# Kernel optimization log

Measured on AMD Instinct MI355X. Metric: run time of the kernel, lower is better.

The kernel has to match this reference:

```python
import jax, jax.numpy as jnp
import numpy as np

ALPHA = 0.2          # LeakyReLU negative slope
NEG_INF = -9e15      # mask value from the torch code
B, N, F, E, H, S, T, L = 32, 128, 78, 12, 256, 20, 13, 3


def setup_inputs() -> dict:
    key = jax.random.key(0)
    ks = jax.random.split(key, 20)
    sc = 0.05  # param scale
    inp = {
        "node_features": jax.random.normal(ks[0], (B, N, F), jnp.float32),
        "edge_features": jax.random.normal(ks[1], (B, N, N, E), jnp.float32),
        "adj_matrix": jax.random.randint(ks[2], (B, N, N), 0, 2).astype(jnp.int32),
        "scaffold_features": jax.random.normal(ks[3], (B, S), jnp.float32),
        # node projection (Linear F->H, with bias)
        "W_node": jax.random.normal(ks[4], (F, H), jnp.float32) * sc,
        "b_node": jnp.zeros((H,), jnp.float32),
        # stacked GAT layer params: W (H->H, no bias), a (2H->1, no bias)
        "gat_W": jax.random.normal(ks[5], (L, H, H), jnp.float32) * sc,
        "gat_a": jax.random.normal(ks[6], (L, 2 * H), jnp.float32) * sc,
        # scaffold projection (S->H)
        "W_sc": jax.random.normal(ks[7], (S, H), jnp.float32) * sc,
        "b_sc": jnp.zeros((H,), jnp.float32),
        # graph_pooling MLP: H -> H/2 -> H/4 (shared for graph + scaffold paths)
        "gp_w1": jax.random.normal(ks[8], (H, H // 2), jnp.float32) * sc,
        "gp_b1": jnp.zeros((H // 2,), jnp.float32),
        "gp_w2": jax.random.normal(ks[9], (H // 2, H // 4), jnp.float32) * sc,
        "gp_b2": jnp.zeros((H // 4,), jnp.float32),
        # output MLP: (H/4 + H/4) -> H/2 -> T
        "out_w1": jax.random.normal(ks[10], (H // 2, H // 2), jnp.float32) * sc,
        "out_b1": jnp.zeros((H // 2,), jnp.float32),
        "out_w2": jax.random.normal(ks[11], (H // 2, T), jnp.float32) * sc,
        "out_b2": jnp.zeros((T,), jnp.float32),
    }
    return inp


def _gat_stack(x, adj_matrix, gat_W, gat_a):
    # x: (B,N,H); adj: (B,N,N) int
    mask = adj_matrix > 0
    n_layers, _, h_dim = gat_W.shape
    for l in range(n_layers):
        h = jnp.einsum("bnf,fh->bnh", x, gat_W[l])      # (B,N,H)
        a1, a2 = gat_a[l, :h_dim], gat_a[l, h_dim:]
        # a . [h_i ; h_j] == h_i.a1 + h_j.a2 (exact decomposition of the
        # O(N^2, 2H) concat in the torch code)
        s1 = h @ a1                                       # (B,N)
        s2 = h @ a2                                       # (B,N)
        e = jax.nn.leaky_relu(s1[:, :, None] + s2[:, None, :], ALPHA)
        att = jnp.where(mask, e, NEG_INF)                 # (B,N,N)
        att = jax.nn.softmax(att, axis=-1)
        h_prime = jnp.einsum("bij,bjh->bih", att, h)
        x = jax.nn.relu(h_prime)                          # relu after layer (dropout = identity, eval)
    return x


def _pool(z, gp_w1, gp_b1, gp_w2, gp_b2):
    z = jax.nn.relu(z @ gp_w1 + gp_b1)
    return jax.nn.relu(z @ gp_w2 + gp_b2)


def reference(node_features, edge_features, adj_matrix, scaffold_features,
              W_node, b_node, gat_W, gat_a, W_sc, b_sc,
              gp_w1, gp_b1, gp_w2, gp_b2, out_w1, out_b1, out_w2, out_b2):
    # edge_features is accepted but unused in the original forward
    x = node_features @ W_node + b_node                  # (B,N,H)
    x = _gat_stack(x, adj_matrix, gat_W, gat_a)
    graph = x.mean(axis=1)                               # (B,H)
    g = _pool(graph, gp_w1, gp_b1, gp_w2, gp_b2)         # (B,H/4)
    s = _pool(scaffold_features @ W_sc + b_sc, gp_w1, gp_b1, gp_w2, gp_b2)
    c = jnp.concatenate([g, s], axis=-1)                 # (B,H/2)
    hdn = jax.nn.relu(c @ out_w1 + out_b1)
    return hdn @ out_w2 + out_b2                         # (B,T)
```

## Files before the change

kernel.cpp:

```cpp
#include <hip/hip_runtime.h>
#include <hip/hip_bf16.h>

#define NEG_INF -9.0e15f

__device__ __forceinline__ float b2f(__hip_bfloat16 v) { return __bfloat162float(v); }
__device__ __forceinline__ float ldv(const float* p, int i) { return p[i]; }
__device__ __forceinline__ float ldv(const __hip_bfloat16* p, int i) { return __bfloat162float(p[i]); }

__device__ __forceinline__ void unpack8u(uint4 r, float* f) {
    f[0]=__uint_as_float(r.x<<16); f[1]=__uint_as_float(r.x&0xffff0000u);
    f[2]=__uint_as_float(r.y<<16); f[3]=__uint_as_float(r.y&0xffff0000u);
    f[4]=__uint_as_float(r.z<<16); f[5]=__uint_as_float(r.z&0xffff0000u);
    f[6]=__uint_as_float(r.w<<16); f[7]=__uint_as_float(r.w&0xffff0000u);
}
__device__ __forceinline__ void ld8f(const float* p, float* f) {
    const float4* q = (const float4*)p;
    float4 a = q[0], b = q[1];
    f[0]=a.x; f[1]=a.y; f[2]=a.z; f[3]=a.w; f[4]=b.x; f[5]=b.y; f[6]=b.z; f[7]=b.w;
}
__device__ __forceinline__ void ld8f(const __hip_bfloat16* p, float* f) {
    unpack8u(*(const uint4*)p, f);
}

__device__ __forceinline__ void async16(const void* g, void* l) {
    __builtin_amdgcn_global_load_lds(
        (__attribute__((address_space(1))) void*)(g),
        (__attribute__((address_space(3))) void*)(l), 16, 0, 0);
}

__device__ __forceinline__ int sniff(const void* wnode) {
    const unsigned short* w = (const unsigned short*)wnode;
    int lane = threadIdx.x & 63;
    unsigned short u = w[2 * lane];
    int e = (u >> 7) & 0xFF;
    unsigned long long m = __ballot(e >= 100 && e <= 140);
    return __popcll(m) >= 48;
}

template <typename T>
__device__ __forceinline__ void gat_epilogue(
    const T* __restrict__ ga, int tx, int ty, int row0,
    const float* acc0, const float* acc1,
    float* __restrict__ h, float* __restrict__ s1, float* __restrict__ s2) {
    float a1v[8], a2v[8];
    ld8f(ga + 8 * tx, a1v);
    ld8f(ga + 256 + 8 * tx, a2v);
    float d10 = 0.f, d20 = 0.f, d11 = 0.f, d21 = 0.f;
    #pragma unroll
    for (int j = 0; j < 8; ++j) {
        d10 += acc0[j] * a1v[j]; d20 += acc0[j] * a2v[j];
        d11 += acc1[j] * a1v[j]; d21 += acc1[j] * a2v[j];
    }
    #pragma unroll
    for (int off = 1; off < 32; off <<= 1) {
        d10 += __shfl_xor(d10, off, 64); d20 += __shfl_xor(d20, off, 64);
        d11 += __shfl_xor(d11, off, 64); d21 += __shfl_xor(d21, off, 64);
    }
    if (tx == 0) {
        s1[row0 + ty] = d10;     s2[row0 + ty] = d20;
        s1[row0 + ty + 8] = d11; s2[row0 + ty + 8] = d21;
    }
    float4 o00 = {acc0[0], acc0[1], acc0[2], acc0[3]};
    float4 o01 = {acc0[4], acc0[5], acc0[6], acc0[7]};
    float4 o10 = {acc1[0], acc1[1], acc1[2], acc1[3]};
    float4 o11 = {acc1[4], acc1[5], acc1[6], acc1[7]};
    *(float4*)&h[(size_t)(row0 + ty) * 256 + 8 * tx]         = o00;
    *(float4*)&h[(size_t)(row0 + ty) * 256 + 8 * tx + 4]     = o01;
    *(float4*)&h[(size_t)(row0 + ty + 8) * 256 + 8 * tx]     = o10;
    *(float4*)&h[(size_t)(row0 + ty + 8) * 256 + 8 * tx + 4] = o11;
}

__global__ __launch_bounds__(256) void k_gat_h(
    const float* __restrict__ x, const void* __restrict__ gat_W,
    const void* __restrict__ gat_a, int layer,
    const void* __restrict__ nf, const void* __restrict__ Wn,
    const void* __restrict__ bn, int first,
    float* __restrict__ h, float* __restrict__ s1, float* __restrict__ s2) {
    __shared__ float xs[16][256];
    __shared__ float nfs[16][80];
    __shared__ __align__(16) unsigned short Wbuf[2][32 * 256];
    const int t = threadIdx.x;
    const int row0 = blockIdx.x * 16;
    const int tx = t & 31, ty = t >> 5;
    const int isbf = sniff(Wn);

    if (isbf) {
        const __hip_bfloat16* Wl = (const __hip_bfloat16*)gat_W + (size_t)layer * 65536;
        const __hip_bfloat16* ga = (const __hip_bfloat16*)gat_a + (size_t)layer * 512;
        const int ph = blockIdx.x & 7;
        {
            const char* g = (const char*)Wl + ph * 16384;
            char* lb = (char*)&Wbuf[0][0];
            #pragma unroll
            for (int i = 0; i < 4; ++i)
                async16(g + i * 4096 + t * 16, lb + i * 4096 + t * 16);
        }
        if (first) {
            for (int idx = t; idx < 16 * 78; idx += 256) {
                int r = idx / 78, k = idx - r * 78;
                nfs[r][k] = b2f(((const __hip_bfloat16*)nf)[(row0 + r) * 78 + k]);
            }
            __syncthreads();
            const __hip_bfloat16* Wnb = (const __hip_bfloat16*)Wn;
            float p0[8], p1[8];
            ld8f((const __hip_bfloat16*)bn + 8 * tx, p0);
            #pragma unroll
            for (int j = 0; j < 8; ++j) p1[j] = p0[j];
            for (int k = 0; k < 78; ++k) {
                float w8[8]; ld8f(Wnb + k * 256 + 8 * tx, w8);
                float xv0 = nfs[ty][k], xv1 = nfs[ty + 8][k];
                #pragma unroll
                for (int j = 0; j < 8; ++j) {
                    p0[j] += xv0 * w8[j];
                    p1[j] += xv1 * w8[j];
                }
            }
            #pragma unroll
            for (int j = 0; j < 8; ++j) {
                xs[ty][8 * tx + j] = p0[j];
                xs[ty + 8][8 * tx + j] = p1[j];
            }
            __syncthreads();
        } else {
            #pragma unroll
            for (int i = 0; i < 4; ++i) {
                int idx = t + 256 * i;
                int r = idx >> 6, c4 = idx & 63;
                ((float4*)&xs[r][0])[c4] = ((const float4*)&x[(size_t)(row0 + r) * 256])[c4];
            }
            __syncthreads();
        }
        float acc0[8], acc1[8];
        #pragma unroll
        for (int j = 0; j < 8; ++j) { acc0[j] = 0.f; acc1[j] = 0.f; }
        for (int c = 0; c < 8; ++c) {
            if (c < 7) {
                const char* g = (const char*)Wl + (((c + 1 + ph) & 7) * 16384);
                char* lb = (char*)&Wbuf[(c + 1) & 1][0];
                #pragma unroll
                for (int i = 0; i < 4; ++i)
                    async16(g + i * 4096 + t * 16, lb + i * 4096 + t * 16);
            }
            const unsigned short* Wc = &Wbuf[c & 1][0];
            const int kb = ((c + ph) & 7) * 32;
            #pragma unroll 2
            for (int k0 = 0; k0 < 32; k0 += 4) {
                float4 xa = *(const float4*)&xs[ty][kb + k0];
                float4 xb = *(const float4*)&xs[ty + 8][kb + k0];
                float xav[4] = {xa.x, xa.y, xa.z, xa.w};
                float xbv[4] = {xb.x, xb.y, xb.z, xb.w};
                #pragma unroll
                for (int kk = 0; kk < 4; ++kk) {
                    uint4 wv = *(const uint4*)&Wc[(k0 + kk) * 256 + 8 * tx];
                    float w8[8]; unpack8u(wv, w8);
                    #pragma unroll
                    for (int j = 0; j < 8; ++j) {
                        acc0[j] += xav[kk] * w8[j];
                        acc1[j] += xbv[kk] * w8[j];
                    }
                }
            }
            __syncthreads();
        }
        gat_epilogue<__hip_bfloat16>(ga, tx, ty, row0, acc0, acc1, h, s1, s2);
    } else {
        const float* Wl = (const float*)gat_W + (size_t)layer * 65536;
        const float* ga = (const float*)gat_a + (size_t)layer * 512;
        if (first) {
            for (int idx = t; idx < 16 * 78; idx += 256) {
                int r = idx / 78, k = idx - r * 78;
                nfs[r][k] = ((const float*)nf)[(row0 + r) * 78 + k];
            }
            __syncthreads();
            float p0[8], p1[8];
            ld8f((const float*)bn + 8 * tx, p0);
            #pragma unroll
            for (int j = 0; j < 8; ++j) p1[j] = p0[j];
            for (int k = 0; k < 78; ++k) {
                float w8[8]; ld8f((const float*)Wn + k * 256 + 8 * tx, w8);
                float xv0 = nfs[ty][k], xv1 = nfs[ty + 8][k];
                #pragma unroll
                for (int j = 0; j < 8; ++j) { p0[j] += xv0 * w8[j]; p1[j] += xv1 * w8[j]; }
            }
            #pragma unroll
            for (int j = 0; j < 8; ++j) {
                xs[ty][8 * tx + j] = p0[j];
                xs[ty + 8][8 * tx + j] = p1[j];
            }
            __syncthreads();
        } else {
            #pragma unroll
            for (int i = 0; i < 4; ++i) {
                int idx = t + 256 * i;
                int r = idx >> 6, c4 = idx & 63;
                ((float4*)&xs[r][0])[c4] = ((const float4*)&x[(size_t)(row0 + r) * 256])[c4];
            }
            __syncthreads();
        }
        float acc0[8], acc1[8];
        #pragma unroll
        for (int j = 0; j < 8; ++j) { acc0[j] = 0.f; acc1[j] = 0.f; }
        for (int k = 0; k < 256; ++k) {
            float w8[8]; ld8f(Wl + k * 256 + 8 * tx, w8);
            float xv0 = xs[ty][k], xv1 = xs[ty + 8][k];
            #pragma unroll
            for (int j = 0; j < 8; ++j) { acc0[j] += xv0 * w8[j]; acc1[j] += xv1 * w8[j]; }
        }
        gat_epilogue<float>(ga, tx, ty, row0, acc0, acc1, h, s1, s2);
    }
}

__global__ __launch_bounds__(256) void k_attn(
    const float* __restrict__ h, const float* __restrict__ s1,
    const float* __restrict__ s2, const int* __restrict__ adj,
    float* __restrict__ x, float* __restrict__ gpart, int do_pool) {
    __shared__ float att_t[128][10];
    __shared__ __align__(16) float hbuf[2][32 * 256];
    __shared__ float pool_red[4][256];
    int blk = blockIdx.x, b = blk >> 4, i0 = (blk & 15) << 3;
    int t = threadIdx.x, w = t >> 6, lane = t & 63;
    const char* hbytes = (const char*)(h + (size_t)b * 32768);
    const int ph = blk & 3;
    {
        char* lb = (char*)&hbuf[0][0];
        const char* g = hbytes + ph * 32768;
        #pragma unroll
        for (int i = 0; i < 8; ++i)
            async16(g + i * 4096 + t * 16, lb + i * 4096 + t * 16);
    }
    {
        int c0 = lane, c1 = lane + 64;
        int ir0 = i0 + 2 * w, ir1 = ir0 + 1;
        const int* a0 = adj + (size_t)(b * 128 + ir0) * 128;
        const int* a1 = adj + (size_t)(b * 128 + ir1) * 128;
        int m00 = a0[c0], m01 = a0[c1], m10 = a1[c0], m11 = a1[c1];
        float sv0 = s1[b * 128 + ir0], sv1 = s1[b * 128 + ir1];
        float t0 = s2[b * 128 + c0],   t1 = s2[b * 128 + c1];
        float e00 = sv0 + t0; e00 = (e00 >= 0.f) ? e00 : 0.2f * e00;
        float e01 = sv0 + t1; e01 = (e01 >= 0.f) ? e01 : 0.2f * e01;
        float e10 = sv1 + t0; e10 = (e10 >= 0.f) ? e10 : 0.2f * e10;
        float e11 = sv1 + t1; e11 = (e11 >= 0.f) ? e11 : 0.2f * e11;
        float v00 = (m00 > 0) ? e00 : NEG_INF;
        float v01 = (m01 > 0) ? e01 : NEG_INF;
        float v10 = (m10 > 0) ? e10 : NEG_INF;
        float v11 = (m11 > 0) ? e11 : NEG_INF;
        float mx0 = fmaxf(v00, v01), mx1 = fmaxf(v10, v11);
        #pragma unroll
        for (int off = 1; off < 64; off <<= 1) {
            mx0 = fmaxf(mx0, __shfl_xor(mx0, off, 64));
            mx1 = fmaxf(mx1, __shfl_xor(mx1, off, 64));
        }
        float p00 = __expf(v00 - mx0), p01 = __expf(v01 - mx0);
        float p10 = __expf(v10 - mx1), p11 = __expf(v11 - mx1);
        float s0 = p00 + p01, ss1 = p10 + p11;
        #pragma unroll
        for (int off = 1; off < 64; off <<= 1) {
            s0  += __shfl_xor(s0, off, 64);
            ss1 += __shfl_xor(ss1, off, 64);
        }
        float inv0 = 1.0f / s0, inv1 = 1.0f / ss1;
        att_t[c0][2 * w]     = p00 * inv0;
        att_t[c1][2 * w]     = p01 * inv0;
        att_t[c0][2 * w + 1] = p10 * inv1;
        att_t[c1][2 * w + 1] = p11 * inv1;
    }
    __syncthreads();
    int tx = t & 63, ty = t >> 6;
    float acc0[4] = {0.f, 0.f, 0.f, 0.f}, acc1[4] = {0.f, 0.f, 0.f, 0.f};
    for (int c = 0; c < 4; ++c) {
        if (c < 3) {
            char* lb = (char*)&hbuf[(c + 1) & 1][0];
            const char* g = hbytes + (((c + 1 + ph) & 3) * 32768);
            #pragma unroll
            for (int i = 0; i < 8; ++i)
                async16(g + i * 4096 + t * 16, lb + i * 4096 + t * 16);
        }
        const float* hc = &hbuf[c & 1][0];
        const int jb = ((c + ph) & 3) * 32;
        #pragma unroll 4
        for (int jj = 0; jj < 32; ++jj) {
            float4 hv = *(const float4*)&hc[jj * 256 + 4 * tx];
            float2 ap = *(const float2*)&att_t[jb + jj][2 * ty];
            acc0[0] += ap.x * hv.x; acc0[1] += ap.x * hv.y;
            acc0[2] += ap.x * hv.z; acc0[3] += ap.x * hv.w;
            acc1[0] += ap.y * hv.x; acc1[1] += ap.y * hv.y;
            acc1[2] += ap.y * hv.z; acc1[3] += ap.y * hv.w;
        }
        __syncthreads();
    }
    if (!do_pool) {
        float4 o0 = {fmaxf(acc0[0],0.f), fmaxf(acc0[1],0.f), fmaxf(acc0[2],0.f), fmaxf(acc0[3],0.f)};
        float4 o1 = {fmaxf(acc1[0],0.f), fmaxf(acc1[1],0.f), fmaxf(acc1[2],0.f), fmaxf(acc1[3],0.f)};
        *(float4*)&x[(size_t)(b * 128 + i0 + 2 * ty)     * 256 + 4 * tx] = o0;
        *(float4*)&x[(size_t)(b * 128 + i0 + 2 * ty + 1) * 256 + 4 * tx] = o1;
    } else {
        float4 pr = {(fmaxf(acc0[0],0.f) + fmaxf(acc1[0],0.f)) * (1.f/128.f),
                     (fmaxf(acc0[1],0.f) + fmaxf(acc1[1],0.f)) * (1.f/128.f),
// ... 130 lines not shown
    }
    __syncthreads();
    if (t < 13) {
        if (isbf) ((__hip_bfloat16*)out)[b * 13 + t] = __float2bfloat16(outv[t]);
        else      ((float*)out)[b * 13 + t] = outv[t];
    }
}

extern "C" void kernel_launch(void* const* d_in, const int* in_sizes, int n_in,
                              void* d_out, int out_size, void* d_ws, size_t ws_size,
                              hipStream_t stream) {
    (void)in_sizes; (void)n_in; (void)out_size; (void)ws_size;
    const void* nf     = d_in[0];
    const int*  adj    = (const int*)d_in[2];
    const void* scaf   = d_in[3];
    const void* W_node = d_in[4];
    const void* b_node = d_in[5];
    const void* gat_W  = d_in[6];
    const void* gat_a  = d_in[7];
    const void* W_sc   = d_in[8];
    const void* b_sc   = d_in[9];
    const void* gp_w1  = d_in[10];
    const void* gp_b1  = d_in[11];
    const void* gp_w2  = d_in[12];
    const void* gp_b2  = d_in[13];
    const void* out_w1 = d_in[14];
    const void* out_b1 = d_in[15];
    const void* out_w2 = d_in[16];
    const void* out_b2 = d_in[17];

    float* ws    = (float*)d_ws;
    float* x     = ws;
    float* h     = ws + 1048576;
    float* s1    = ws + 2097152;
    float* s2    = s1 + 4096;
    float* gpart = s2 + 4096;

    for (int l = 0; l < 3; ++l) {
        k_gat_h<<<256, 256, 0, stream>>>(x, gat_W, gat_a, l,
                                         nf, W_node, b_node, (l == 0) ? 1 : 0,
                                         h, s1, s2);
        k_attn<<<512, 256, 0, stream>>>(h, s1, s2, adj, x, gpart, (l == 2) ? 1 : 0);
    }
    k_head<<<32, 256, 0, stream>>>(gpart, scaf, W_sc, b_sc, gp_w1, gp_b1, gp_w2, gp_b2,
                                   out_w1, out_b1, out_w2, out_b2, d_out, W_node);
}
```

Baseline: 228.2 us.

## Use bf16 MFMA with hi/lo split for GAT projection and node embedding

Replaces the scalar FMA projection x@W in the GAT kernel with MFMA 16x16x32 bf16 instructions. Activations are split into bf16 hi and lo parts so that fp32-level accuracy is kept, and the node embedding also runs on MFMA. A new pre-pass kernel transposes the layer and node weights into an N-major layout so they can be fed to the MFMA. The grid is doubled by splitting the output columns into two halves, and the partial attention scores are summed in the attention kernel. This adds an extra launch plus transpose work, and uses two MFMAs per tile.

```diff
diff --git a/kernel.cpp b/kernel.cpp
--- a/kernel.cpp
+++ b/kernel.cpp
@@ -2,25 +2,32 @@
 #include <hip/hip_bf16.h>
 
 #define NEG_INF -9.0e15f
+
+using u16 = unsigned short;
+typedef float f32x4 __attribute__((ext_vector_type(4)));
+typedef short s16x8 __attribute__((ext_vector_type(8)));
 
 __device__ __forceinline__ float b2f(__hip_bfloat16 v) { return __bfloat162float(v); }
 __device__ __forceinline__ float ldv(const float* p, int i) { return p[i]; }
 __device__ __forceinline__ float ldv(const __hip_bfloat16* p, int i) { return __bfloat162float(p[i]); }
-
-__device__ __forceinline__ void unpack8u(uint4 r, float* f) {
+__device__ __forceinline__ float bu2f(u16 u) { return __uint_as_float(((unsigned)u) << 16); }
+__device__ __forceinline__ u16 f2bu(float v) {
+    __hip_bfloat16 h = __float2bfloat16(v);
+    return *(u16*)&h;
+}
+
+__device__ __forceinline__ void ld8f(const float* p, float* f) {
+    const float4* q = (const float4*)p;
+    float4 a = q[0], b = q[1];
+    f[0]=a.x; f[1]=a.y; f[2]=a.z; f[3]=a.w; f[4]=b.x; f[5]=b.y; f[6]=b.z; f[7]=b.w;
+}
+__device__ __forceinline__ void ld8f(const __hip_bfloat16* p, float* f) {
+    uint4 r = *(const uint4*)p;
     f[0]=__uint_as_float(r.x<<16); f[1]=__uint_as_float(r.x&0xffff0000u);
     f[2]=__uint_as_float(r.y<<16); f[3]=__uint_as_float(r.y&0xffff0000u);
     f[4]=__uint_as_float(r.z<<16); f[5]=__uint_as_float(r.z&0xffff0000u);
     f[6]=__uint_as_float(r.w<<16); f[7]=__uint_as_float(r.w&0xffff0000u);
 }
-__device__ __forceinline__ void ld8f(const float* p, float* f) {
-    const float4* q = (const float4*)p;
-    float4 a = q[0], b = q[1];
-    f[0]=a.x; f[1]=a.y; f[2]=a.z; f[3]=a.w; f[4]=b.x; f[5]=b.y; f[6]=b.z; f[7]=b.w;
-}
-__device__ __forceinline__ void ld8f(const __hip_bfloat16* p, float* f) {
-    unpack8u(*(const uint4*)p, f);
-}
 
 __device__ __forceinline__ void async16(const void* g, void* l) {
     __builtin_amdgcn_global_load_lds(
@@ -28,191 +35,268 @@
         (__attribute__((address_space(3))) void*)(l), 16, 0, 0);
 }
 
+__device__ __forceinline__ f32x4 mfma16(s16x8 a, s16x8 b, f32x4 c) {
+    return __builtin_amdgcn_mfma_f32_16x16x32_bf16(a, b, c, 0, 0, 0);
+}
+
 __device__ __forceinline__ int sniff(const void* wnode) {
-    const unsigned short* w = (const unsigned short*)wnode;
+    const u16* w = (const u16*)wnode;
     int lane = threadIdx.x & 63;
-    unsigned short u = w[2 * lane];
+    u16 u = w[2 * lane];
     int e = (u >> 7) & 0xFF;
     unsigned long long m = __ballot(e >= 100 && e <= 140);
     return __popcll(m) >= 48;
 }
 
-template <typename T>
-__device__ __forceinline__ void gat_epilogue(
-    const T* __restrict__ ga, int tx, int ty, int row0,
-    const float* acc0, const float* acc1,
-    float* __restrict__ h, float* __restrict__ s1, float* __restrict__ s2) {
-    float a1v[8], a2v[8];
-    ld8f(ga + 8 * tx, a1v);
-    ld8f(ga + 256 + 8 * tx, a2v);
-    float d10 = 0.f, d20 = 0.f, d11 = 0.f, d21 = 0.f;
-    #pragma unroll
-    for (int j = 0; j < 8; ++j) {
-        d10 += acc0[j] * a1v[j]; d20 += acc0[j] * a2v[j];
-        d11 += acc1[j] * a1v[j]; d21 += acc1[j] * a2v[j];
-    }
-    #pragma unroll
-    for (int off = 1; off < 32; off <<= 1) {
-        d10 += __shfl_xor(d10, off, 64); d20 += __shfl_xor(d20, off, 64);
-        d11 += __shfl_xor(d11, off, 64); d21 += __shfl_xor(d21, off, 64);
-    }
-    if (tx == 0) {
-        s1[row0 + ty] = d10;     s2[row0 + ty] = d20;
-        s1[row0 + ty + 8] = d11; s2[row0 + ty + 8] = d21;
-    }
-    float4 o00 = {acc0[0], acc0[1], acc0[2], acc0[3]};
-    float4 o01 = {acc0[4], acc0[5], acc0[6], acc0[7]};
-    float4 o10 = {acc1[0], acc1[1], acc1[2], acc1[3]};
-    float4 o11 = {acc1[4], acc1[5], acc1[6], acc1[7]};
-    *(float4*)&h[(size_t)(row0 + ty) * 256 + 8 * tx]         = o00;
-    *(float4*)&h[(size_t)(row0 + ty) * 256 + 8 * tx + 4]     = o01;
-    *(float4*)&h[(size_t)(row0 + ty + 8) * 256 + 8 * tx]     = o10;
-    *(float4*)&h[(size_t)(row0 + ty + 8) * 256 + 8 * tx + 4] = o11;
-}
-
-__global__ __launch_bounds__(256) void k_gat_h(
-    const float* __restrict__ x, const void* __restrict__ gat_W,
-    const void* __restrict__ gat_a, int layer,
-    const void* __restrict__ nf, const void* __restrict__ Wn,
-    const void* __restrict__ bn, int first,
-    float* __restrict__ h, float* __restrict__ s1, float* __restrict__ s2) {
-    __shared__ float xs[16][256];
-    __shared__ float nfs[16][80];
-    __shared__ __align__(16) unsigned short Wbuf[2][32 * 256];
+__global__ __launch_bounds__(256) void k_wt(
+    const void* __restrict__ gat_W, const void* __restrict__ W_node,
+    u16* __restrict__ Wt, u16* __restrict__ Wnt) {
+    if (!sniff(W_node)) return;
+    int b = blockIdx.x, t = threadIdx.x;
+    if (b < 24) {
+        int l = b >> 3, nb = (b & 7) * 32;
+        const u16* Ws = (const u16*)gat_W + (size_t)l * 65536;
+        u16* Wd = Wt + (size_t)l * 65536;
+        int n = nb + (t & 31), kc = t >> 5;
+        u16 tmp[32];
+        #pragma unroll 8
+        for (int kk = 0; kk < 32; ++kk) tmp[kk] = Ws[(kc * 32 + kk) * 256 + n];
+        #pragma unroll
+        for (int kk = 0; kk < 32; ++kk) Wd[n * 256 + kc * 32 + kk] = tmp[kk];
+    } else {
+        int nb = (b - 24) * 128;
+        const u16* Ws = (const u16*)W_node;
+        int n = nb + (t >> 1), hf = t & 1;
+        for (int kk = 0; kk < 48; ++kk) {
+            int k = hf * 48 + kk;
+            Wnt[n * 96 + k] = (k < 78) ? Ws[k * 256 + n] : (u16)0;
+        }
+    }
+}
+
+__global__ __launch_bounds__(256) void k_gat(
+    const float* __restrict__ x, const u16* __restrict__ Wt,
+    const void* __restrict__ gat_W_raw, const void* __restrict__ gat_a,
+    int layer, const void* __restrict__ nf, const u16* __restrict__ Wnt,
+    const void* __restrict__ Wn_raw, const void* __restrict__ bn, int first,
+    float* __restrict__ h, float* __restrict__ sp1, float* __restrict__ sp2) {
+    __shared__ __align__(16) char smem[36864];
+    u16* xs_hi = (u16*)smem;
+    u16* xs_lo = (u16*)(smem + 8448);
+    char* wbB  = smem + 16896;
+    u16* nfs   = (u16*)(smem + 33280);
+    float* sred = (float*)(smem + 36352);
+
     const int t = threadIdx.x;
-    const int row0 = blockIdx.x * 16;
-    const int tx = t & 31, ty = t >> 5;
-    const int isbf = sniff(Wn);
+    const int w = t >> 6, lane = t & 63, quad = lane >> 4, l16 = lane & 15;
+    const int rb = blockIdx.x >> 1, nh = blockIdx.x & 1;
+    const int row0 = rb * 16, n0 = nh * 128;
+    const int isbf = sniff(Wn_raw);
 
     if (isbf) {
-        const __hip_bfloat16* Wl = (const __hip_bfloat16*)gat_W + (size_t)layer * 65536;
-        const __hip_bfloat16* ga = (const __hip_bfloat16*)gat_a + (size_t)layer * 512;
-        const int ph = blockIdx.x & 7;
+        if (first) {
+            const u16* nfu = (const u16*)nf;
+            for (int i = t; i < 16 * 96; i += 256) {
+                int r = i / 96, k = i - r * 96;
+                nfs[i] = (k < 78) ? nfu[(row0 + r) * 78 + k] : (u16)0;
+            }
+            __syncthreads();
+            f32x4 pa[4];
+            const u16* bnu = (const u16*)bn;
+            #pragma unroll
+            for (int tt = 0; tt < 4; ++tt) {
+                float bv = bu2f(bnu[w * 64 + tt * 16 + l16]);
+                pa[tt] = (f32x4){bv, bv, bv, bv};
+            }
+            for (int c = 0; c < 3; ++c) {
+                #pragma unroll
+                for (int j = 0; j < 4; ++j) {
+                    int dest = (w * 4 + j) * 4096 + lane * 16;
+                    int nl = (w * 4 + j) * 64 + (lane >> 2);
+                    const char* src = (const char*)(Wnt + nl * 96 + c * 32 + (lane & 3) * 8);
+                    async16(src, wbB + dest);
+                }
+                __syncthreads();
+                s16x8 a = *(const s16x8*)(nfs + l16 * 96 + c * 32 + quad * 8);
+                #pragma unroll
+                for (int tt = 0; tt < 4; ++tt) {
+                    s16x8 bfr = *(const s16x8*)((const u16*)wbB +
+                                 (w * 64 + tt * 16 + l16) * 32 + quad * 8);
+                    pa[tt] = mfma16(a, bfr, pa[tt]);
+                }
+                __syncthreads();
+            }
+            #pragma unroll
+            for (int tt = 0; tt < 4; ++tt) {
+                #pragma unroll
+                for (int r = 0; r < 4; ++r) {
+                    float v = pa[tt][r];
+                    u16 hi = f2bu(v);
+                    u16 lo = f2bu(v - bu2f(hi));
+                    int idx = (quad * 4 + r) * 264 + w * 64 + tt * 16 + l16;
+                    xs_hi[idx] = hi;
+                    xs_lo[idx] = lo;
+                }
+            }
+        } else {
+            int row = t >> 4, kb = (t & 15) * 16;
+            const float4* xp = (const float4*)(x + (size_t)(row0 + row) * 256 + kb);
+            float v[16];
+            #pragma unroll
+            for (int q = 0; q < 4; ++q) {
+                float4 f = xp[q];
+                v[4*q] = f.x; v[4*q+1] = f.y; v[4*q+2] = f.z; v[4*q+3] = f.w;
+            }
+            unsigned hp[8], lp[8];
+            #pragma unroll
+            for (int i = 0; i < 8; ++i) {
+                u16 h0 = f2bu(v[2*i]),   h1 = f2bu(v[2*i+1]);
+                u16 l0 = f2bu(v[2*i] - bu2f(h0)), l1 = f2bu(v[2*i+1] - bu2f(h1));
+                hp[i] = (unsigned)h0 | ((unsigned)h1 << 16);
+                lp[i] = (unsigned)l0 | ((unsigned)l1 << 16);
+            }
+            uint4* dh = (uint4*)(xs_hi + row * 264 + kb);
+            uint4* dl = (uint4*)(xs_lo + row * 264 + kb);
+            dh[0] = (uint4){hp[0], hp[1], hp[2], hp[3]};
+            dh[1] = (uint4){hp[4], hp[5], hp[6], hp[7]};
+            dl[0] = (uint4){lp[0], lp[1], lp[2], lp[3]};
+            dl[1] = (uint4){lp[4], lp[5], lp[6], lp[7]};
+        }
+        const u16* Wtl = Wt + (size_t)layer * 65536;
         {
-            const char* g = (const char*)Wl + ph * 16384;
-            char* lb = (char*)&Wbuf[0][0];
-            #pragma unroll
-            for (int i = 0; i < 4; ++i)
-                async16(g + i * 4096 + t * 16, lb + i * 4096 + t * 16);
-        }
+            #pragma unroll
+            for (int j = 0; j < 2; ++j) {
+                int dest = (w * 2 + j) * 2048 + lane * 16;
+                int nl = (w * 2 + j) * 32 + (lane >> 2);
+                const char* src = (const char*)(Wtl + (size_t)(n0 + nl) * 256 + (lane & 3) * 8);
+                async16(src, wbB + dest);
+            }
+        }
+        f32x4 ac0 = {0.f, 0.f, 0.f, 0.f}, ac1 = {0.f, 0.f, 0.f, 0.f};
+        for (int c = 0; c < 8; ++c) {
+            __syncthreads();
+            if (c < 7) {
+                #pragma unroll
+                for (int j = 0; j < 2; ++j) {
+                    int dest = (((c + 1) & 1) * 8192) + (w * 2 + j) * 2048 + lane * 16;
+                    int nl = (w * 2 + j) * 32 + (lane >> 2);
+                    const char* src = (const char*)(Wtl + (size_t)(n0 + nl) * 256 +
+                                                    (c + 1) * 32 + (lane & 3) * 8);
+                    async16(src, wbB + dest);
+                }
+            }
+            const u16* wb = (const u16*)(wbB + (c & 1) * 8192);
+            s16x8 ah = *(const s16x8*)(xs_hi + l16 * 264 + c * 32 + quad * 8);
+            s16x8 al = *(const s16x8*)(xs_lo + l16 * 264 + c * 32 + quad * 8);
+            s16x8 b0 = *(const s16x8*)(wb + (w * 32 + l16) * 32 + quad * 8);
+            s16x8 b1 = *(const s16x8*)(wb + (w * 32 + 16 + l16) * 32 + quad * 8);
+            ac0 = mfma16(ah, b0, ac0);
+            ac0 = mfma16(al, b0, ac0);
+            ac1 = mfma16(ah, b1, ac1);
+            ac1 = mfma16(al, b1, ac1);
+        }
+        const __hip_bfloat16* gab = (const __hip_bfloat16*)gat_a + (size_t)layer * 512;
+        int c0 = n0 + w * 32 + l16, c1 = c0 + 16;
+        float a10 = b2f(gab[c0]), a11 = b2f(gab[c1]);
+        float a20 = b2f(gab[256 + c0]), a21 = b2f(gab[256 + c1]);
+        float p1[4], p2[4];
+        #pragma unroll
+        for (int r = 0; r < 4; ++r) {
+            p1[r] = ac0[r] * a10 + ac1[r] * a11;
+            p2[r] = ac0[r] * a20 + ac1[r] * a21;
+            #pragma unroll
+            for (int off = 1; off < 16; off <<= 1) {
+                p1[r] += __shfl_xor(p1[r], off, 64);
+                p2[r] += __shfl_xor(p2[r], off, 64);
+            }
+        }
+        if (l16 == 0) {
+            #pragma unroll
+            for (int r = 0; r < 4; ++r) {
+                sred[w * 16 + quad * 4 + r] = p1[r];
+                sred[64 + w * 16 + quad * 4 + r] = p2[r];
+            }
+        }
+        #pragma unroll
+        for (int r = 0; r < 4; ++r) {
+            int gr = row0 + quad * 4 + r;
+            h[(size_t)gr * 256 + n0 + w * 32 + l16]      = ac0[r];
+            h[(size_t)gr * 256 + n0 + w * 32 + 16 + l16] = ac1[r];
+        }
+        __syncthreads();
+        if (t < 16) {
+            sp1[nh * 4096 + row0 + t] = sred[t] + sred[16 + t] + sred[32 + t] + sred[48 + t];
+            sp2[nh * 4096 + row0 + t] = sred[64 + t] + sred[80 + t] + sred[96 + t] + sred[112 + t];
+        }
+    } else {
+        float* xsf = (float*)smem;
+        const float* Wl = (const float*)gat_W_raw + (size_t)layer * 65536;
+        const float* gaf = (const float*)gat_a + (size_t)layer * 512;
         if (first) {
-            for (int idx = t; idx < 16 * 78; idx += 256) {
-                int r = idx / 78, k = idx - r * 78;
-                nfs[r][k] = b2f(((const __hip_bfloat16*)nf)[(row0 + r) * 78 + k]);
+            float* nfsf = (float*)(smem + 16896);
+            const float* nff = (const float*)nf;
+            for (int i = t; i < 16 * 78; i += 256) {
+                int r = i / 78, k = i - r * 78;
+                nfsf[r * 80 + k] = nff[(row0 + r) * 78 + k];
             }
             __syncthreads();
-            const __hip_bfloat16* Wnb = (const __hip_bfloat16*)Wn;
-            float p0[8], p1[8];
-            ld8f((const __hip_bfloat16*)bn + 8 * tx, p0);
-            #pragma unroll
-            for (int j = 0; j < 8; ++j) p1[j] = p0[j];
+            int row = t >> 4, cb = (t & 15) * 16;
+            const float* Wnf = (const float*)Wn_raw;
+            const float* bnf = (const float*)bn;
+            float acc[16];
+            #pragma unroll
+            for (int j = 0; j < 16; ++j) acc[j] = bnf[cb + j];
             for (int k = 0; k < 78; ++k) {
-                float w8[8]; ld8f(Wnb + k * 256 + 8 * tx, w8);
-                float xv0 = nfs[ty][k], xv1 = nfs[ty + 8][k];
+                float xv = nfsf[row * 80 + k];
                 #pragma unroll
-                for (int j = 0; j < 8; ++j) {
-                    p0[j] += xv0 * w8[j];
-                    p1[j] += xv1 * w8[j];
-                }
-            }
-            #pragma unroll
-            for (int j = 0; j < 8; ++j) {
-                xs[ty][8 * tx + j] = p0[j];
-                xs[ty + 8][8 * tx + j] = p1[j];
-            }
+                for (int j = 0; j < 16; ++j) acc[j] += xv * Wnf[k * 256 + cb + j];
+            }
+            #pragma unroll
+            for (int j = 0; j < 16; ++j) xsf[row * 256 + cb + j] = acc[j];
             __syncthreads();
         } else {
-            #pragma unroll
-            for (int i = 0; i < 4; ++i) {
-                int idx = t + 256 * i;
-                int r = idx >> 6, c4 = idx & 63;
-                ((float4*)&xs[r][0])[c4] = ((const float4*)&x[(size_t)(row0 + r) * 256])[c4];
+            for (int i = t; i < 16 * 64; i += 256) {
+                int r = i >> 6, c4 = i & 63;
+                ((float4*)(xsf + r * 256))[c4] =
+                    ((const float4*)(x + (size_t)(row0 + r) * 256))[c4];
             }
             __syncthreads();
         }
-        float acc0[8], acc1[8];
-        #pragma unroll
-        for (int j = 0; j < 8; ++j) { acc0[j] = 0.f; acc1[j] = 0.f; }
-        for (int c = 0; c < 8; ++c) {
-            if (c < 7) {
-                const char* g = (const char*)Wl + (((c + 1 + ph) & 7) * 16384);
-                char* lb = (char*)&Wbuf[(c + 1) & 1][0];
-                #pragma unroll
-                for (int i = 0; i < 4; ++i)
-                    async16(g + i * 4096 + t * 16, lb + i * 4096 + t * 16);
-            }
-            const unsigned short* Wc = &Wbuf[c & 1][0];
-            const int kb = ((c + ph) & 7) * 32;
-            #pragma unroll 2
-            for (int k0 = 0; k0 < 32; k0 += 4) {
-                float4 xa = *(const float4*)&xs[ty][kb + k0];
-                float4 xb = *(const float4*)&xs[ty + 8][kb + k0];
-                float xav[4] = {xa.x, xa.y, xa.z, xa.w};
-                float xbv[4] = {xb.x, xb.y, xb.z, xb.w};
-                #pragma unroll
-                for (int kk = 0; kk < 4; ++kk) {
-                    uint4 wv = *(const uint4*)&Wc[(k0 + kk) * 256 + 8 * tx];
-                    float w8[8]; unpack8u(wv, w8);
-                    #pragma unroll
-                    for (int j = 0; j < 8; ++j) {
-                        acc0[j] += xav[kk] * w8[j];
-                        acc1[j] += xbv[kk] * w8[j];
-                    }
-                }
-            }
-            __syncthreads();
-        }
-        gat_epilogue<__hip_bfloat16>(ga, tx, ty, row0, acc0, acc1, h, s1, s2);
-    } else {
-        const float* Wl = (const float*)gat_W + (size_t)layer * 65536;
-        const float* ga = (const float*)gat_a + (size_t)layer * 512;
-        if (first) {
-            for (int idx = t; idx < 16 * 78; idx += 256) {
-                int r = idx / 78, k = idx - r * 78;
-                nfs[r][k] = ((const float*)nf)[(row0 + r) * 78 + k];
-            }
-            __syncthreads();
-            float p0[8], p1[8];
-            ld8f((const float*)bn + 8 * tx, p0);
-            #pragma unroll
-            for (int j = 0; j < 8; ++j) p1[j] = p0[j];
-            for (int k = 0; k < 78; ++k) {
-                float w8[8]; ld8f((const float*)Wn + k * 256 + 8 * tx, w8);
-                float xv0 = nfs[ty][k], xv1 = nfs[ty + 8][k];
-                #pragma unroll
-                for (int j = 0; j < 8; ++j) { p0[j] += xv0 * w8[j]; p1[j] += xv1 * w8[j]; }
-            }
-            #pragma unroll
-            for (int j = 0; j < 8; ++j) {
-                xs[ty][8 * tx + j] = p0[j];
-                xs[ty + 8][8 * tx + j] = p1[j];
-            }
-            __syncthreads();
-        } else {
-            #pragma unroll
-            for (int i = 0; i < 4; ++i) {
-                int idx = t + 256 * i;
-                int r = idx >> 6, c4 = idx & 63;
-                ((float4*)&xs[r][0])[c4] = ((const float4*)&x[(size_t)(row0 + r) * 256])[c4];
-            }
-            __syncthreads();
-        }
-        float acc0[8], acc1[8];
-        #pragma unroll
-        for (int j = 0; j < 8; ++j) { acc0[j] = 0.f; acc1[j] = 0.f; }
+        int ty = t >> 4, col0 = n0 + (t & 15) * 8;
+        float acc[8];
+        #pragma unroll
+        for (int j = 0; j < 8; ++j) acc[j] = 0.f;
         for (int k = 0; k < 256; ++k) {
-            float w8[8]; ld8f(Wl + k * 256 + 8 * tx, w8);
-            float xv0 = xs[ty][k], xv1 = xs[ty + 8][k];
-            #pragma unroll
-            for (int j = 0; j < 8; ++j) { acc0[j] += xv0 * w8[j]; acc1[j] += xv1 * w8[j]; }
-        }
-        gat_epilogue<float>(ga, tx, ty, row0, acc0, acc1, h, s1, s2);
+            float xv = xsf[ty * 256 + k];
+            float w8[8]; ld8f(Wl + k * 256 + col0, w8);
+            #pragma unroll
+            for (int j = 0; j < 8; ++j) acc[j] += xv * w8[j];
+        }
+        float d1 = 0.f, d2 = 0.f;
+        #pragma unroll
+        for (int j = 0; j < 8; ++j) {
+            d1 += acc[j] * gaf[col0 + j];
+            d2 += acc[j] * gaf[256 + col0 + j];
+        }
+        #pragma unroll
+        for (int off = 1; off < 16; off <<= 1) {
+            d1 += __shfl_xor(d1, off, 64);
+            d2 += __shfl_xor(d2, off, 64);
+        }
+        if ((lane & 15) == 0) { sred[ty] = d1; sred[32 + ty] = d2; }
+        #pragma unroll
+        for (int j = 0; j < 8; ++j) h[(size_t)(row0 + ty) * 256 + col0 + j] = acc[j];
+        __syncthreads();
+        if (t < 16) {
+            sp1[nh * 4096 + row0 + t] = sred[t];
+            sp2[nh * 4096 + row0 + t] = sred[32 + t];
+        }
     }
 }
 
 __global__ __launch_bounds__(256) void k_attn(
-    const float* __restrict__ h, const float* __restrict__ s1,
-    const float* __restrict__ s2, const int* __restrict__ adj,
+    const float* __restrict__ h, const float* __restrict__ sp1,
+    const float* __restrict__ sp2, const int* __restrict__ adj,
     float* __restrict__ x, float* __restrict__ gpart, int do_pool) {
     __shared__ float att_t[128][10];
     __shared__ __align__(16) float hbuf[2][32 * 256];
@@ -234,8 +318,10 @@
         const int* a0 = adj + (size_t)(b * 128 + ir0) * 128;
         const int* a1 = adj + (size_t)(b * 128 + ir1) * 128;
         int m00 = a0[c0], m01 = a0[c1], m10 = a1[c0], m11 = a1[c1];
-        float sv0 = s1[b * 128 + ir0], sv1 = s1[b * 128 + ir1];
-        float t0 = s2[b * 128 + c0],   t1 = s2[b * 128 + c1];
+        float sv0 = sp1[b * 128 + ir0] + sp1[4096 + b * 128 + ir0];
+        float sv1 = sp1[b * 128 + ir1] + sp1[4096 + b * 128 + ir1];
+        float t0 = sp2[b * 128 + c0] + sp2[4096 + b * 128 + c0];
+        float t1 = sp2[b * 128 + c1] + sp2[4096 + b * 128 + c1];
         float e00 = sv0 + t0; e00 = (e00 >= 0.f) ? e00 : 0.2f * e00;
         float e01 = sv0 + t1; e01 = (e01 >= 0.f) ? e01 : 0.2f * e01;
         float e10 = sv1 + t0; e10 = (e10 >= 0.f) ? e10 : 0.2f * e10;
@@ -459,15 +545,18 @@
     float* ws    = (float*)d_ws;
     float* x     = ws;
     float* h     = ws + 1048576;
-    float* s1    = ws + 2097152;
-    float* s2    = s1 + 4096;
-    float* gpart = s2 + 4096;
-
+    float* sp1   = ws + 2097152;
+    float* sp2   = sp1 + 8192;
+    float* gpart = sp2 + 8192;
+    u16*   Wt    = (u16*)(gpart + 131072);
+    u16*   Wnt   = Wt + 196608;
+
+    k_wt<<<26, 256, 0, stream>>>(gat_W, W_node, Wt, Wnt);
     for (int l = 0; l < 3; ++l) {
-        k_gat_h<<<256, 256, 0, stream>>>(x, gat_W, gat_a, l,
-                                         nf, W_node, b_node, (l == 0) ? 1 : 0,
-                                         h, s1, s2);
-        k_attn<<<512, 256, 0, stream>>>(h, s1, s2, adj, x, gpart, (l == 2) ? 1 : 0);
+        k_gat<<<512, 256, 0, stream>>>(x, Wt, gat_W, gat_a, l,
+                                       nf, Wnt, W_node, b_node, (l == 0) ? 1 : 0,
+                                       h, sp1, sp2);
+        k_attn<<<512, 256, 0, stream>>>(h, sp1, sp2, adj, x, gpart, (l == 2) ? 1 : 0);
     }
     k_head<<<32, 256, 0, stream>>>(gpart, scaf, W_sc, b_sc, gp_w1, gp_b1, gp_w2, gp_b2,
                                    out_w1, out_b1, out_w2, out_b2, d_out, W_node);
```

Measured after the change: 285.2 us. +25.0%, slower.

## Replicate bf16 weights into 8 copies and shrink GAT projection tiles to 8 rows

Applied to the files above, without the earlier changes.

Adds a kernel that copies gat_W and W_node into eight replicated buffers in workspace, so that blocks read from different copies (selected by bx&7) and contention on the same addresses is reduced. The projection kernel now handles 8 rows per block across 512 blocks and streams weights straight from global memory instead of double-buffering them in LDS through async loads. Activations are stored transposed in shared memory. Costs are one extra launch with a copy every call, and each weight value is reused over fewer rows, so each block issues more global reads.

```diff
diff --git a/kernel.cpp b/kernel.cpp
--- a/kernel.cpp
+++ b/kernel.cpp
@@ -2,25 +2,12 @@
 #include <hip/hip_bf16.h>
 
 #define NEG_INF -9.0e15f
+
+using u16 = unsigned short;
 
 __device__ __forceinline__ float b2f(__hip_bfloat16 v) { return __bfloat162float(v); }
 __device__ __forceinline__ float ldv(const float* p, int i) { return p[i]; }
 __device__ __forceinline__ float ldv(const __hip_bfloat16* p, int i) { return __bfloat162float(p[i]); }
-
-__device__ __forceinline__ void unpack8u(uint4 r, float* f) {
-    f[0]=__uint_as_float(r.x<<16); f[1]=__uint_as_float(r.x&0xffff0000u);
-    f[2]=__uint_as_float(r.y<<16); f[3]=__uint_as_float(r.y&0xffff0000u);
-    f[4]=__uint_as_float(r.z<<16); f[5]=__uint_as_float(r.z&0xffff0000u);
-    f[6]=__uint_as_float(r.w<<16); f[7]=__uint_as_float(r.w&0xffff0000u);
-}
-__device__ __forceinline__ void ld8f(const float* p, float* f) {
-    const float4* q = (const float4*)p;
-    float4 a = q[0], b = q[1];
-    f[0]=a.x; f[1]=a.y; f[2]=a.z; f[3]=a.w; f[4]=b.x; f[5]=b.y; f[6]=b.z; f[7]=b.w;
-}
-__device__ __forceinline__ void ld8f(const __hip_bfloat16* p, float* f) {
-    unpack8u(*(const uint4*)p, f);
-}
 
 __device__ __forceinline__ void async16(const void* g, void* l) {
     __builtin_amdgcn_global_load_lds(
@@ -29,184 +16,191 @@
 }
 
 __device__ __forceinline__ int sniff(const void* wnode) {
-    const unsigned short* w = (const unsigned short*)wnode;
+    const u16* w = (const u16*)wnode;
     int lane = threadIdx.x & 63;
-    unsigned short u = w[2 * lane];
+    u16 u = w[2 * lane];
     int e = (u >> 7) & 0xFF;
     unsigned long long m = __ballot(e >= 100 && e <= 140);
     return __popcll(m) >= 48;
 }
 
-template <typename T>
-__device__ __forceinline__ void gat_epilogue(
-    const T* __restrict__ ga, int tx, int ty, int row0,
-    const float* acc0, const float* acc1,
+__global__ __launch_bounds__(256) void k_rep(
+    const void* __restrict__ gat_W, const void* __restrict__ W_node,
+    u16* __restrict__ Wrep, u16* __restrict__ Wnrep) {
+    if (!sniff(W_node)) return;
+    int b = blockIdx.x, t = threadIdx.x;
+    if (b < 384) {
+        int c = b / 48, idx = (b % 48) * 256 + t;
+        ((uint4*)(Wrep + (size_t)c * 196608))[idx] = ((const uint4*)gat_W)[idx];
+    } else {
+        int bb = b - 384;
+        int c = bb / 5, idx = (bb % 5) * 256 + t;
+        if (idx < 1248)
+            ((uint4*)(Wnrep + (size_t)c * 19968))[idx] = ((const uint4*)W_node)[idx];
+    }
+}
+
+__global__ __launch_bounds__(256) void k_gat(
+    const float* __restrict__ x, const void* __restrict__ gat_W,
+    const u16* __restrict__ Wrep, const void* __restrict__ gat_a, int layer,
+    const void* __restrict__ nf, const void* __restrict__ Wn_raw,
+    const u16* __restrict__ Wnrep, const void* __restrict__ bn, int first,
     float* __restrict__ h, float* __restrict__ s1, float* __restrict__ s2) {
-    float a1v[8], a2v[8];
-    ld8f(ga + 8 * tx, a1v);
-    ld8f(ga + 256 + 8 * tx, a2v);
-    float d10 = 0.f, d20 = 0.f, d11 = 0.f, d21 = 0.f;
-    #pragma unroll
-    for (int j = 0; j < 8; ++j) {
-        d10 += acc0[j] * a1v[j]; d20 += acc0[j] * a2v[j];
-        d11 += acc1[j] * a1v[j]; d21 += acc1[j] * a2v[j];
-    }
-    #pragma unroll
-    for (int off = 1; off < 32; off <<= 1) {
-        d10 += __shfl_xor(d10, off, 64); d20 += __shfl_xor(d20, off, 64);
-        d11 += __shfl_xor(d11, off, 64); d21 += __shfl_xor(d21, off, 64);
-    }
-    if (tx == 0) {
-        s1[row0 + ty] = d10;     s2[row0 + ty] = d20;
-        s1[row0 + ty + 8] = d11; s2[row0 + ty + 8] = d21;
-    }
-    float4 o00 = {acc0[0], acc0[1], acc0[2], acc0[3]};
-    float4 o01 = {acc0[4], acc0[5], acc0[6], acc0[7]};
-    float4 o10 = {acc1[0], acc1[1], acc1[2], acc1[3]};
-    float4 o11 = {acc1[4], acc1[5], acc1[6], acc1[7]};
-    *(float4*)&h[(size_t)(row0 + ty) * 256 + 8 * tx]         = o00;
-    *(float4*)&h[(size_t)(row0 + ty) * 256 + 8 * tx + 4]     = o01;
-    *(float4*)&h[(size_t)(row0 + ty + 8) * 256 + 8 * tx]     = o10;
-    *(float4*)&h[(size_t)(row0 + ty + 8) * 256 + 8 * tx + 4] = o11;
-}
-
-__global__ __launch_bounds__(256) void k_gat_h(
-    const float* __restrict__ x, const void* __restrict__ gat_W,
-    const void* __restrict__ gat_a, int layer,
-    const void* __restrict__ nf, const void* __restrict__ Wn,
-    const void* __restrict__ bn, int first,
-    float* __restrict__ h, float* __restrict__ s1, float* __restrict__ s2) {
-    __shared__ float xs[16][256];
-    __shared__ float nfs[16][80];
-    __shared__ __align__(16) unsigned short Wbuf[2][32 * 256];
+    __shared__ float xsT[256 * 10];
     const int t = threadIdx.x;
-    const int row0 = blockIdx.x * 16;
-    const int tx = t & 31, ty = t >> 5;
-    const int isbf = sniff(Wn);
+    const int bx = blockIdx.x;
+    const int row0 = bx * 8;
+    const int tx = t & 63, w = t >> 6;
+    const int isbf = sniff(Wn_raw);
+    const int c0 = 4 * tx;
+
+    float acc0[4], acc1[4];
 
     if (isbf) {
-        const __hip_bfloat16* Wl = (const __hip_bfloat16*)gat_W + (size_t)layer * 65536;
+        if (first) {
+            const u16* nfu = (const u16*)nf;
+            for (int i = t; i < 624; i += 256) {
+                int r = i / 78, k = i - r * 78;
+                xsT[k * 10 + r] = __uint_as_float(((unsigned)nfu[(row0 + r) * 78 + k]) << 16);
+            }
+            __syncthreads();
+            const u16* Wnl = Wnrep + (size_t)(bx & 7) * 19968;
+            const __hip_bfloat16* bnb = (const __hip_bfloat16*)bn;
+            #pragma unroll
+            for (int j = 0; j < 4; ++j) { acc0[j] = b2f(bnb[c0 + j]); acc1[j] = acc0[j]; }
+            #pragma unroll 2
+            for (int k = 0; k < 78; ++k) {
+                uint2 wv = *(const uint2*)(Wnl + k * 256 + c0);
+                float w0 = __uint_as_float(wv.x << 16);
+                float w1 = __uint_as_float(wv.x & 0xffff0000u);
+                float w2 = __uint_as_float(wv.y << 16);
+                float w3 = __uint_as_float(wv.y & 0xffff0000u);
+                float2 xp = *(const float2*)&xsT[k * 10 + 2 * w];
+                acc0[0] += xp.x * w0; acc0[1] += xp.x * w1;
+                acc0[2] += xp.x * w2; acc0[3] += xp.x * w3;
+                acc1[0] += xp.y * w0; acc1[1] += xp.y * w1;
+                acc1[2] += xp.y * w2; acc1[3] += xp.y * w3;
+            }
+            __syncthreads();
+            #pragma unroll
+            for (int j = 0; j < 4; ++j) {
+                xsT[(c0 + j) * 10 + 2 * w]     = acc0[j];
+                xsT[(c0 + j) * 10 + 2 * w + 1] = acc1[j];
+            }
+            __syncthreads();
+        } else {
+            int r = t >> 5, cb = (t & 31) * 8;
+            const float4* xp = (const float4*)(x + (size_t)(row0 + r) * 256 + cb);
+            float4 f0 = xp[0], f1 = xp[1];
+            xsT[(cb + 0) * 10 + r] = f0.x; xsT[(cb + 1) * 10 + r] = f0.y;
+            xsT[(cb + 2) * 10 + r] = f0.z; xsT[(cb + 3) * 10 + r] = f0.w;
+            xsT[(cb + 4) * 10 + r] = f1.x; xsT[(cb + 5) * 10 + r] = f1.y;
+            xsT[(cb + 6) * 10 + r] = f1.z; xsT[(cb + 7) * 10 + r] = f1.w;
+            __syncthreads();
+        }
+        const u16* Wl = Wrep + (size_t)(bx & 7) * 196608 + (size_t)layer * 65536;
+        #pragma unroll
+        for (int j = 0; j < 4; ++j) { acc0[j] = 0.f; acc1[j] = 0.f; }
+        #pragma unroll 4
+        for (int k = 0; k < 256; ++k) {
+            uint2 wv = *(const uint2*)(Wl + k * 256 + c0);
+            float w0 = __uint_as_float(wv.x << 16);
+            float w1 = __uint_as_float(wv.x & 0xffff0000u);
+            float w2 = __uint_as_float(wv.y << 16);
+            float w3 = __uint_as_float(wv.y & 0xffff0000u);
+            float2 xp = *(const float2*)&xsT[k * 10 + 2 * w];
+            acc0[0] += xp.x * w0; acc0[1] += xp.x * w1;
+            acc0[2] += xp.x * w2; acc0[3] += xp.x * w3;
+            acc1[0] += xp.y * w0; acc1[1] += xp.y * w1;
+            acc1[2] += xp.y * w2; acc1[3] += xp.y * w3;
+        }
         const __hip_bfloat16* ga = (const __hip_bfloat16*)gat_a + (size_t)layer * 512;
-        const int ph = blockIdx.x & 7;
-        {
-            const char* g = (const char*)Wl + ph * 16384;
-            char* lb = (char*)&Wbuf[0][0];
+        float d10 = 0.f, d20 = 0.f, d11 = 0.f, d21 = 0.f;
+        #pragma unroll
+        for (int j = 0; j < 4; ++j) {
+            float a1v = b2f(ga[c0 + j]), a2v = b2f(ga[256 + c0 + j]);
+            d10 += acc0[j] * a1v; d20 += acc0[j] * a2v;
+            d11 += acc1[j] * a1v; d21 += acc1[j] * a2v;
+        }
+        #pragma unroll
+        for (int off = 1; off < 64; off <<= 1) {
+            d10 += __shfl_xor(d10, off, 64); d20 += __shfl_xor(d20, off, 64);
+            d11 += __shfl_xor(d11, off, 64); d21 += __shfl_xor(d21, off, 64);
+        }
+        if (tx == 0) {
+            s1[row0 + 2 * w] = d10;     s2[row0 + 2 * w] = d20;
+            s1[row0 + 2 * w + 1] = d11; s2[row0 + 2 * w + 1] = d21;
+        }
+        *(float4*)&h[(size_t)(row0 + 2 * w) * 256 + c0]     = (float4){acc0[0], acc0[1], acc0[2], acc0[3]};
+        *(float4*)&h[(size_t)(row0 + 2 * w + 1) * 256 + c0] = (float4){acc1[0], acc1[1], acc1[2], acc1[3]};
+    } else {
+        const float* Wlf = (const float*)gat_W + (size_t)layer * 65536;
+        const float* gaf = (const float*)gat_a + (size_t)layer * 512;
+        if (first) {
+            const float* nff = (const float*)nf;
+            for (int i = t; i < 624; i += 256) {
+                int r = i / 78, k = i - r * 78;
+                xsT[k * 10 + r] = nff[(row0 + r) * 78 + k];
+            }
+            __syncthreads();
+            const float* Wnf = (const float*)Wn_raw;
+            const float* bnf = (const float*)bn;
             #pragma unroll
-            for (int i = 0; i < 4; ++i)
-                async16(g + i * 4096 + t * 16, lb + i * 4096 + t * 16);
-        }
-        if (first) {
-            for (int idx = t; idx < 16 * 78; idx += 256) {
-                int r = idx / 78, k = idx - r * 78;
-                nfs[r][k] = b2f(((const __hip_bfloat16*)nf)[(row0 + r) * 78 + k]);
-            }
-            __syncthreads();
-            const __hip_bfloat16* Wnb = (const __hip_bfloat16*)Wn;
-            float p0[8], p1[8];
-            ld8f((const __hip_bfloat16*)bn + 8 * tx, p0);
+            for (int j = 0; j < 4; ++j) { acc0[j] = bnf[c0 + j]; acc1[j] = acc0[j]; }
+            for (int k = 0; k < 78; ++k) {
+                float4 wf = *(const float4*)(Wnf + k * 256 + c0);
+                float2 xp = *(const float2*)&xsT[k * 10 + 2 * w];
+                acc0[0] += xp.x * wf.x; acc0[1] += xp.x * wf.y;
+                acc0[2] += xp.x * wf.z; acc0[3] += xp.x * wf.w;
+                acc1[0] += xp.y * wf.x; acc1[1] += xp.y * wf.y;
+                acc1[2] += xp.y * wf.z; acc1[3] += xp.y * wf.w;
+            }
+            __syncthreads();
             #pragma unroll
-            for (int j = 0; j < 8; ++j) p1[j] = p0[j];
-            for (int k = 0; k < 78; ++k) {
-                float w8[8]; ld8f(Wnb + k * 256 + 8 * tx, w8);
-                float xv0 = nfs[ty][k], xv1 = nfs[ty + 8][k];
-                #pragma unroll
-                for (int j = 0; j < 8; ++j) {
-                    p0[j] += xv0 * w8[j];
-                    p1[j] += xv1 * w8[j];
-                }
-            }
-            #pragma unroll
-            for (int j = 0; j < 8; ++j) {
-                xs[ty][8 * tx + j] = p0[j];
-                xs[ty + 8][8 * tx + j] = p1[j];
+            for (int j = 0; j < 4; ++j) {
+                xsT[(c0 + j) * 10 + 2 * w]     = acc0[j];
+                xsT[(c0 + j) * 10 + 2 * w + 1] = acc1[j];
             }
             __syncthreads();
         } else {
-            #pragma unroll
-            for (int i = 0; i < 4; ++i) {
-                int idx = t + 256 * i;
-                int r = idx >> 6, c4 = idx & 63;
-                ((float4*)&xs[r][0])[c4] = ((const float4*)&x[(size_t)(row0 + r) * 256])[c4];
-            }
-            __syncthreads();
-        }
-        float acc0[8], acc1[8];
-        #pragma unroll
-        for (int j = 0; j < 8; ++j) { acc0[j] = 0.f; acc1[j] = 0.f; }
-        for (int c = 0; c < 8; ++c) {
-            if (c < 7) {
-                const char* g = (const char*)Wl + (((c + 1 + ph) & 7) * 16384);
-                char* lb = (char*)&Wbuf[(c + 1) & 1][0];
-                #pragma unroll
-                for (int i = 0; i < 4; ++i)
-                    async16(g + i * 4096 + t * 16, lb + i * 4096 + t * 16);
-            }
-            const unsigned short* Wc = &Wbuf[c & 1][0];
-            const int kb = ((c + ph) & 7) * 32;
-            #pragma unroll 2
-            for (int k0 = 0; k0 < 32; k0 += 4) {
-                float4 xa = *(const float4*)&xs[ty][kb + k0];
-                float4 xb = *(const float4*)&xs[ty + 8][kb + k0];
-                float xav[4] = {xa.x, xa.y, xa.z, xa.w};
-                float xbv[4] = {xb.x, xb.y, xb.z, xb.w};
-                #pragma unroll
-                for (int kk = 0; kk < 4; ++kk) {
-                    uint4 wv = *(const uint4*)&Wc[(k0 + kk) * 256 + 8 * tx];
-                    float w8[8]; unpack8u(wv, w8);
-                    #pragma unroll
-                    for (int j = 0; j < 8; ++j) {
-                        acc0[j] += xav[kk] * w8[j];
-                        acc1[j] += xbv[kk] * w8[j];
-                    }
-                }
-            }
-            __syncthreads();
-        }
-        gat_epilogue<__hip_bfloat16>(ga, tx, ty, row0, acc0, acc1, h, s1, s2);
-    } else {
-        const float* Wl = (const float*)gat_W + (size_t)layer * 65536;
-        const float* ga = (const float*)gat_a + (size_t)layer * 512;
-        if (first) {
-            for (int idx = t; idx < 16 * 78; idx += 256) {
-                int r = idx / 78, k = idx - r * 78;
-                nfs[r][k] = ((const float*)nf)[(row0 + r) * 78 + k];
-            }
-            __syncthreads();
-            float p0[8], p1[8];
-            ld8f((const float*)bn + 8 * tx, p0);
-            #pragma unroll
-            for (int j = 0; j < 8; ++j) p1[j] = p0[j];
-            for (int k = 0; k < 78; ++k) {
-                float w8[8]; ld8f((const float*)Wn + k * 256 + 8 * tx, w8);
-                float xv0 = nfs[ty][k], xv1 = nfs[ty + 8][k];
-                #pragma unroll
-                for (int j = 0; j < 8; ++j) { p0[j] += xv0 * w8[j]; p1[j] += xv1 * w8[j]; }
-            }
-            #pragma unroll
-            for (int j = 0; j < 8; ++j) {
-                xs[ty][8 * tx + j] = p0[j];
-                xs[ty + 8][8 * tx + j] = p1[j];
-            }
-            __syncthreads();
-        } else {
-            #pragma unroll
-            for (int i = 0; i < 4; ++i) {
-                int idx = t + 256 * i;
-                int r = idx >> 6, c4 = idx & 63;
-                ((float4*)&xs[r][0])[c4] = ((const float4*)&x[(size_t)(row0 + r) * 256])[c4];
-            }
-            __syncthreads();
-        }
-        float acc0[8], acc1[8];
-        #pragma unroll
-        for (int j = 0; j < 8; ++j) { acc0[j] = 0.f; acc1[j] = 0.f; }
+            int r = t >> 5, cb = (t & 31) * 8;
+            const float4* xp = (const float4*)(x + (size_t)(row0 + r) * 256 + cb);
+            float4 f0 = xp[0], f1 = xp[1];
+            xsT[(cb + 0) * 10 + r] = f0.x; xsT[(cb + 1) * 10 + r] = f0.y;
+            xsT[(cb + 2) * 10 + r] = f0.z; xsT[(cb + 3) * 10 + r] = f0.w;
+            xsT[(cb + 4) * 10 + r] = f1.x; xsT[(cb + 5) * 10 + r] = f1.y;
+            xsT[(cb + 6) * 10 + r] = f1.z; xsT[(cb + 7) * 10 + r] = f1.w;
+            __syncthreads();
+        }
+        #pragma unroll
+        for (int j = 0; j < 4; ++j) { acc0[j] = 0.f; acc1[j] = 0.f; }
+        #pragma unroll 4
         for (int k = 0; k < 256; ++k) {
-            float w8[8]; ld8f(Wl + k * 256 + 8 * tx, w8);
-            float xv0 = xs[ty][k], xv1 = xs[ty + 8][k];
-            #pragma unroll
-            for (int j = 0; j < 8; ++j) { acc0[j] += xv0 * w8[j]; acc1[j] += xv1 * w8[j]; }
-        }
-        gat_epilogue<float>(ga, tx, ty, row0, acc0, acc1, h, s1, s2);
+            float4 wf = *(const float4*)(Wlf + k * 256 + c0);
+            float2 xp = *(const float2*)&xsT[k * 10 + 2 * w];
+            acc0[0] += xp.x * wf.x; acc0[1] += xp.x * wf.y;
+            acc0[2] += xp.x * wf.z; acc0[3] += xp.x * wf.w;
+            acc1[0] += xp.y * wf.x; acc1[1] += xp.y * wf.y;
+            acc1[2] += xp.y * wf.z; acc1[3] += xp.y * wf.w;
+        }
+        float d10 = 0.f, d20 = 0.f, d11 = 0.f, d21 = 0.f;
+        #pragma unroll
+        for (int j = 0; j < 4; ++j) {
+            float a1v = gaf[c0 + j], a2v = gaf[256 + c0 + j];
+            d10 += acc0[j] * a1v; d20 += acc0[j] * a2v;
+            d11 += acc1[j] * a1v; d21 += acc1[j] * a2v;
+        }
+        #pragma unroll
+        for (int off = 1; off < 64; off <<= 1) {
+            d10 += __shfl_xor(d10, off, 64); d20 += __shfl_xor(d20, off, 64);
+            d11 += __shfl_xor(d11, off, 64); d21 += __shfl_xor(d21, off, 64);
+        }
+        if (tx == 0) {
+            s1[row0 + 2 * w] = d10;     s2[row0 + 2 * w] = d20;
+            s1[row0 + 2 * w + 1] = d11; s2[row0 + 2 * w + 1] = d21;
+        }
+        *(float4*)&h[(size_t)(row0 + 2 * w) * 256 + c0]     = (float4){acc0[0], acc0[1], acc0[2], acc0[3]};
+        *(float4*)&h[(size_t)(row0 + 2 * w + 1) * 256 + c0] = (float4){acc1[0], acc1[1], acc1[2], acc1[3]};
     }
 }
 
@@ -229,13 +223,13 @@
             async16(g + i * 4096 + t * 16, lb + i * 4096 + t * 16);
     }
     {
-        int c0 = lane, c1 = lane + 64;
+        int cc0 = lane, cc1 = lane + 64;
         int ir0 = i0 + 2 * w, ir1 = ir0 + 1;
         const int* a0 = adj + (size_t)(b * 128 + ir0) * 128;
         const int* a1 = adj + (size_t)(b * 128 + ir1) * 128;
-        int m00 = a0[c0], m01 = a0[c1], m10 = a1[c0], m11 = a1[c1];
+        int m00 = a0[cc0], m01 = a0[cc1], m10 = a1[cc0], m11 = a1[cc1];
         float sv0 = s1[b * 128 + ir0], sv1 = s1[b * 128 + ir1];
-        float t0 = s2[b * 128 + c0],   t1 = s2[b * 128 + c1];
+        float t0 = s2[b * 128 + cc0],  t1 = s2[b * 128 + cc1];
         float e00 = sv0 + t0; e00 = (e00 >= 0.f) ? e00 : 0.2f * e00;
         float e01 = sv0 + t1; e01 = (e01 >= 0.f) ? e01 : 0.2f * e01;
         float e10 = sv1 + t0; e10 = (e10 >= 0.f) ? e10 : 0.2f * e10;
@@ -259,10 +253,10 @@
             ss1 += __shfl_xor(ss1, off, 64);
         }
         float inv0 = 1.0f / s0, inv1 = 1.0f / ss1;
-        att_t[c0][2 * w]     = p00 * inv0;
-        att_t[c1][2 * w]     = p01 * inv0;
-        att_t[c0][2 * w + 1] = p10 * inv1;
-        att_t[c1][2 * w + 1] = p11 * inv1;
+        att_t[cc0][2 * w]     = p00 * inv0;
+        att_t[cc1][2 * w]     = p01 * inv0;
+        att_t[cc0][2 * w + 1] = p10 * inv1;
+        att_t[cc1][2 * w + 1] = p11 * inv1;
     }
     __syncthreads();
     int tx = t & 63, ty = t >> 6;
@@ -462,11 +456,14 @@
     float* s1    = ws + 2097152;
     float* s2    = s1 + 4096;
     float* gpart = s2 + 4096;
-
+    u16*   Wrep  = (u16*)(gpart + 131072);
+    u16*   Wnrep = Wrep + 8 * 196608;
+
+    k_rep<<<424, 256, 0, stream>>>(gat_W, W_node, Wrep, Wnrep);
     for (int l = 0; l < 3; ++l) {
-        k_gat_h<<<256, 256, 0, stream>>>(x, gat_W, gat_a, l,
-                                         nf, W_node, b_node, (l == 0) ? 1 : 0,
-                                         h, s1, s2);
+        k_gat<<<512, 256, 0, stream>>>(x, gat_W, Wrep, gat_a, l,
+                                       nf, W_node, Wnrep, b_node, (l == 0) ? 1 : 0,
+                                       h, s1, s2);
         k_attn<<<512, 256, 0, stream>>>(h, s1, s2, adj, x, gpart, (l == 2) ? 1 : 0);
     }
     k_head<<<32, 256, 0, stream>>>(gpart, scaf, W_sc, b_sc, gp_w1, gp_b1, gp_w2, gp_b2,
```

Result: no change. 227.2 us (-0.5%).
